# Optimization experiments

Measured on AMD Instinct MI355X. Metric: run time of the kernel, lower is better.

Reference implementation:

```python
import jax, jax.numpy as jnp
import numpy as np

N_NODES = 100000
N_EDGES = 1600000
IN_F = 128
OUT_F = 64
K = 2


def _propagate(x, src, dst, num_nodes):
    """GCN propagation with self-loops already appended to (src, dst).
    out[j] = sum_{(i->j)} deg(i)^-1/2 * deg(j)^-1/2 * x[i]
    where deg is the in-degree counting self-loops (PyG gcn_norm)."""
    deg = jnp.zeros((num_nodes,), dtype=x.dtype).at[dst].add(1.0)
    dinv = jnp.where(deg > 0, jax.lax.rsqrt(deg), 0.0)
    norm = dinv[src] * dinv[dst]                      # [E+N]
    msg = x[src] * norm[:, None]                      # gather + scale
    return jnp.zeros_like(x).at[dst].add(msg)         # scatter-add


def setup_inputs() -> dict:
    key = jax.random.key(0)
    k1, k2, k3, k4 = jax.random.split(key, 4)
    x = jax.random.normal(k1, (N_NODES, IN_F), dtype=jnp.float32)
    edge_index = jax.random.randint(k2, (2, N_EDGES), 0, N_NODES, dtype=jnp.int64)
    # Linear weights, torch convention: y = x @ W.T, W is [out, in]
    W1 = jax.random.normal(k3, (IN_F, IN_F), dtype=jnp.float32) / np.sqrt(IN_F)
    W2 = jax.random.normal(k4, (OUT_F, IN_F), dtype=jnp.float32) / np.sqrt(IN_F)
    return {"x": x, "edge_index": edge_index, "W1": W1, "W2": W2}


def reference(x, edge_index, W1, W2):
    num_nodes = x.shape[0]
    # add self loops once (same augmented edge set used by P1 and P2)
    loop = jnp.arange(num_nodes, dtype=edge_index.dtype)
    src = jnp.concatenate([edge_index[0], loop])
    dst = jnp.concatenate([edge_index[1], loop])
    for _ in range(K):
        x = x @ W1.T
        x = _propagate(x, src, dst, num_nodes)
    x = x @ W2.T
    x = _propagate(x, src, dst, num_nodes)
    # original computes log_softmax into `out` but returns pre-softmax x
    return x
```

## Files before the change

### kernel.cpp

```cpp
#include <hip/hip_runtime.h>

#define NN 100000
#define NE 1600000
#define ENT (NE + NN)
#define NB 196
#define BINCAP 10240


__global__ void probe_zero(const unsigned* __restrict__ edges, int* __restrict__ flag,
                           int* __restrict__ binCnt) {
    int t = threadIdx.x;
    if (t < NB) binCnt[t] = 0;
    if (t == 0) {
        int is64 = 1;
        for (int i = 1; i < 64; i += 2)
            if (edges[i] != 0u) { is64 = 0; break; }
        *flag = is64;
    }
}


__global__ __launch_bounds__(256) void part_kernel(const void* __restrict__ edges,
                                                   const int* __restrict__ flag,
                                                   int* __restrict__ binned,
                                                   int* __restrict__ binCnt) {
    __shared__ int hist[NB], base[NB], rank[NB];
    int t = threadIdx.x;
    for (int i = t; i < NB; i += 256) hist[i] = 0;
    __syncthreads();
    int i0 = blockIdx.x * 4096;
    bool is64 = (*flag != 0);
    int s[16], d[16];
    #pragma unroll
    for (int q = 0; q < 16; ++q) {
        int i = i0 + q * 256 + t;
        if (i < NE) {
            if (is64) {
                s[q] = (int)__builtin_nontemporal_load(&((const long long*)edges)[i]);
                d[q] = (int)__builtin_nontemporal_load(&((const long long*)edges)[NE + i]);
            } else {
                s[q] = __builtin_nontemporal_load(&((const int*)edges)[i]);
                d[q] = __builtin_nontemporal_load(&((const int*)edges)[NE + i]);
            }
            atomicAdd(&hist[d[q] >> 9], 1);
        } else d[q] = -1;
    }
    __syncthreads();
    for (int i = t; i < NB; i += 256) {
        base[i] = atomicAdd(&binCnt[i], hist[i]);
        rank[i] = 0;
    }
    __syncthreads();
    #pragma unroll
    for (int q = 0; q < 16; ++q) {
        if (d[q] >= 0) {
            int b = d[q] >> 9;
            int r = base[b] + atomicAdd(&rank[b], 1);
            if (r < BINCAP)
                binned[(size_t)b * BINCAP + r] = ((d[q] & 511) << 17) | s[q];
        }
    }
}


__global__ __launch_bounds__(1024) void build2_kernel(const int* __restrict__ binCnt,
                                                      const int* __restrict__ binned,
                                                      float* __restrict__ dinv,
                                                      int* __restrict__ rowoff,
                                                      int* __restrict__ edge) {
    extern __shared__ char smem[];
    int* stage = (int*)smem;
    int* hist  = (int*)(smem + (size_t)BINCAP * 4);
    int* sc    = hist + 512;
    int* cur   = sc + 512;
    int* bsc   = cur + 512;
    int b = blockIdx.x, t = threadIdx.x;
    int nb0 = b << 9;
    int nNodes = min(512, NN - nb0);

    if (t < 256) {
        int nodes = (t < NB) ? min(512, NN - (t << 9)) : 0;
        bsc[t] = (t < NB) ? binCnt[t] + nodes : 0;
    }
    if (t < 512) hist[t] = 0;
    __syncthreads();
    for (int off = 1; off < 256; off <<= 1) {
        int a = (t < 256 && t >= off) ? bsc[t - off] : 0;
        __syncthreads();
        if (t < 256) bsc[t] += a;
        __syncthreads();
    }
    int cntRaw = binCnt[b];
    int cnt = min(cntRaw, BINCAP);
    int off0 = bsc[b] - (cntRaw + nNodes);

    const int* e = binned + (size_t)b * BINCAP;
    for (int i = t; i < cnt; i += 1024) atomicAdd(&hist[e[i] >> 17], 1);
    __syncthreads();
    int v = 0;
    if (t < 512) { v = (t < nNodes) ? hist[t] + 1 : 0; sc[t] = v; }
    __syncthreads();
    for (int off = 1; off < 512; off <<= 1) {
        int a = (t < 512 && t >= off) ? sc[t - off] : 0;
        __syncthreads();
        if (t < 512) sc[t] += a;
        __syncthreads();
    }
    if (t < nNodes) {
        dinv[nb0 + t] = rsqrtf((float)(hist[t] + 1));
        int lo = sc[t] - v;
        rowoff[nb0 + t] = off0 + lo;
        stage[lo] = nb0 + t;
        cur[t] = lo + 1;
    }
    if (b == NB - 1 && t == 0) rowoff[NN] = ENT;
    __syncthreads();
    for (int i = t; i < cnt; i += 1024) {
        int pk = e[i];
        int slot = atomicAdd(&cur[pk >> 17], 1);
        if (slot < BINCAP) stage[slot] = pk & 0x1FFFF;
    }
    __syncthreads();
    int total = min(cntRaw + nNodes, BINCAP);
    int* dst = edge + off0;
    for (int i = t; i < total; i += 1024) dst[i] = stage[i];
}


__global__ __launch_bounds__(256) void wprod1_kernel(const float* __restrict__ W1,
                                                     const float* __restrict__ W2,
                                                     float* __restrict__ T) {
    int idx = blockIdx.x * blockDim.x + threadIdx.x;
    if (idx >= 128 * 64) return;
    int k = idx >> 6, j = idx & 63;
    float s = 0.f;
    #pragma unroll 8
    for (int q = 0; q < 128; ++q)
        s += W1[q * 128 + k] * W2[j * 128 + q];
    T[k * 64 + j] = s;
}

__global__ __launch_bounds__(256) void wprod2_kernel(const float* __restrict__ W1,
                                                     const float* __restrict__ T,
                                                     float* __restrict__ WcT) {
    int idx = blockIdx.x * blockDim.x + threadIdx.x;
    if (idx >= 128 * 64) return;
    int i = idx >> 6, j = idx & 63;
    float s = 0.f;
    #pragma unroll 8
    for (int k = 0; k < 128; ++k)
        s += W1[k * 128 + i] * T[k * 64 + j];
    WcT[j * 128 + i] = s;
}


template<int SPOW>
__global__ __launch_bounds__(256) void spmm64f_kernel(const int* __restrict__ rowoff,
                                                      const int* __restrict__ col,
                                                      const float* __restrict__ dinv,
                                                      const float* __restrict__ H,
                                                      float* __restrict__ O) {
    int w = (int)((blockIdx.x * (unsigned)blockDim.x + threadIdx.x) >> 6);
    if (w >= NN) return;
    int lane = threadIdx.x & 63;
    int s = __builtin_amdgcn_readfirstlane(rowoff[w]);
    int e = __builtin_amdgcn_readfirstlane(rowoff[w + 1]);
    float acc = 0.f;
    const float* base = H + lane;

    int p = s;
    for (; p + 8 <= e; p += 8) {
        int c[8];
        #pragma unroll
        for (int q = 0; q < 8; ++q) c[q] = __builtin_nontemporal_load(&col[p + q]);
        #pragma unroll
        for (int q = 0; q < 8; ++q) acc += base[(size_t)c[q] * 64];
    }
    if (p + 4 <= e) {
        int c[4];
        #pragma unroll
        for (int q = 0; q < 4; ++q) c[q] = __builtin_nontemporal_load(&col[p + q]);
        #pragma unroll
        for (int q = 0; q < 4; ++q) acc += base[(size_t)c[q] * 64];
        p += 4;
    }
    for (; p < e; ++p) acc += base[(size_t)__builtin_nontemporal_load(&col[p]) * 64];

    float di = dinv[w];
    float scale = (SPOW == 2) ? di * di : di;
    __builtin_nontemporal_store(acc * scale, &O[(size_t)w * 64 + lane]);
}


__global__ __launch_bounds__(256) void gemm_xwt64_kernel(const float* __restrict__ X,
                                                         const float* __restrict__ W,
                                                         const float* __restrict__ dinv,
                                                         float* __restrict__ Y, int M) {
    constexpr int N = 64, K = 128, BM = 64, BK = 32;
    constexpr int TM = 4, TN = N / 16;
    __shared__ float Xs[BK][BM + 4];
    __shared__ float Ws[BK][N + 4];
    int t  = threadIdx.x;
    int m0 = blockIdx.x * BM;
    int r0 = (t >> 4) * TM;
    int c0 = (t & 15) * TN;
    float acc[TM][TN] = {};
    for (int k0 = 0; k0 < K; k0 += BK) {
        #pragma unroll
        for (int i = 0; i < 2; ++i) {
            int f  = t + i * 256;
            int m  = f >> 3;
            int kq = (f & 7) << 2;
            int gm = m0 + m; if (gm >= M) gm = M - 1;
            float4 v = *(const float4*)&X[(size_t)gm * K + k0 + kq];
            Xs[kq + 0][m] = v.x; Xs[kq + 1][m] = v.y;
            Xs[kq + 2][m] = v.z; Xs[kq + 3][m] = v.w;
        }
        #pragma unroll
        for (int i = 0; i < N / 32; ++i) {
            int f  = t + i * 256;
            int n  = f >> 3;
            int kq = (f & 7) << 2;
            float4 v = *(const float4*)&W[(size_t)n * K + k0 + kq];
            Ws[kq + 0][n] = v.x; Ws[kq + 1][n] = v.y;
            Ws[kq + 2][n] = v.z; Ws[kq + 3][n] = v.w;
        }
        __syncthreads();
        #pragma unroll
        for (int k = 0; k < BK; ++k) {
            float4 xv = *(const float4*)&Xs[k][r0];
            float xf[TM] = {xv.x, xv.y, xv.z, xv.w};
            float wf[TN];
            #pragma unroll
            for (int j = 0; j < TN; j += 4) {
                float4 wv = *(const float4*)&Ws[k][c0 + j];
                wf[j] = wv.x; wf[j + 1] = wv.y; wf[j + 2] = wv.z; wf[j + 3] = wv.w;
            }
            #pragma unroll
            for (int i = 0; i < TM; ++i)
                #pragma unroll
                for (int j = 0; j < TN; ++j)
                    acc[i][j] += xf[i] * wf[j];
        }
        __syncthreads();
    }
    #pragma unroll
    for (int i = 0; i < TM; ++i) {
        int gm = m0 + r0 + i;
        if (gm < M) {
            float di = dinv[gm];
            #pragma unroll
            for (int j = 0; j < TN; j += 4) {
                float4 v = {di * acc[i][j], di * acc[i][j + 1],
                            di * acc[i][j + 2], di * acc[i][j + 3]};
                *(float4*)&Y[(size_t)gm * N + c0 + j] = v;
            }
        }
    }
}


extern "C" void kernel_launch(void* const* d_in, const int* in_sizes, int n_in,
                              void* d_out, int out_size, void* d_ws, size_t ws_size,
                              hipStream_t stream) {
    const float* x     = (const float*)d_in[0];
    const void*  edges = d_in[1];
    const float* W1    = (const float*)d_in[2];
    const float* W2    = (const float*)d_in[3];
    float* out = (float*)d_out;

    char* ws = (char*)d_ws;
    size_t off = 0;
    auto take = [&](size_t bytes) -> char* {
        char* p = ws + off;
        off = (off + bytes + 255) & ~(size_t)255;
        return p;
    };
    int*   flag   = (int*)take(4);
    int*   binCnt = (int*)take((size_t)NB * 4);
    float* dinv   = (float*)take((size_t)NN * 4);
    int*   rowoff = (int*)take((size_t)(NN + 1) * 4);
    float* Tbuf   = (float*)take((size_t)128 * 64 * 4);
    float* WcT    = (float*)take((size_t)64 * 128 * 4);
    int*   binned = (int*)take((size_t)NB * BINCAP * 4);
    int*   edgeA  = (int*)take((size_t)ENT * 4);
    float* g      = (float*)take((size_t)NN * 64 * 4);
    float* y      = (float*)take((size_t)NN * 64 * 4);
    if (off > ws_size) return;

    probe_zero<<<1, 256, 0, stream>>>((const unsigned*)edges, flag, binCnt);
    wprod1_kernel<<<32, 256, 0, stream>>>(W1, W2, Tbuf);
    wprod2_kernel<<<32, 256, 0, stream>>>(W1, Tbuf, WcT);
    part_kernel<<<(NE + 4095) / 4096, 256, 0, stream>>>(edges, flag, binned, binCnt);
    size_t b2lds = (size_t)BINCAP * 4 + (512 * 3 + 256) * 4;
    build2_kernel<<<NB, 1024, b2lds, stream>>>(binCnt, binned, dinv, rowoff, edgeA);

    const int GB = (NN + 63) / 64;
    const int PB = (NN * 64 + 255) / 256;

    gemm_xwt64_kernel<<<GB, 256, 0, stream>>>(x, WcT, dinv, g, NN);
    spmm64f_kernel<2><<<PB, 256, 0, stream>>>(rowoff, edgeA, dinv, g, y);
    spmm64f_kernel<2><<<PB, 256, 0, stream>>>(rowoff, edgeA, dinv, y, g);
    spmm64f_kernel<1><<<PB, 256, 0, stream>>>(rowoff, edgeA, dinv, g, out);
}
```

Baseline: 262.8 us.

## Fuse setup kernels, deepen SpMM unroll, use nontemporal GEMM loads/stores

Merges the probe/zeroing kernel into the first weight-product kernel and folds the second weight product into the tail of the partition kernel, removing two launches. The SpMM row loop is unrolled to 16 gathers in flight, and the GEMM switches its X loads and Y stores to nontemporal scalar accesses. Splitting the float4 accesses into scalars may cost vectorization, and running the weight product inside the partition kernel lengthens a few of its blocks.

```diff
diff --git a/kernel.cpp b/kernel.cpp
--- a/kernel.cpp
+++ b/kernel.cpp
@@ -7,23 +7,40 @@
 #define BINCAP 10240
 
 
-__global__ void probe_zero(const unsigned* __restrict__ edges, int* __restrict__ flag,
-                           int* __restrict__ binCnt) {
-    int t = threadIdx.x;
-    if (t < NB) binCnt[t] = 0;
-    if (t == 0) {
-        int is64 = 1;
-        for (int i = 1; i < 64; i += 2)
-            if (edges[i] != 0u) { is64 = 0; break; }
-        *flag = is64;
-    }
+__global__ __launch_bounds__(256) void wprod1_kernel(const float* __restrict__ W1,
+                                                     const float* __restrict__ W2,
+                                                     float* __restrict__ T,
+                                                     const unsigned* __restrict__ edges,
+                                                     int* __restrict__ flag,
+                                                     int* __restrict__ binCnt) {
+    if (blockIdx.x == 0) {
+        int t = threadIdx.x;
+        if (t < NB) binCnt[t] = 0;
+        if (t == 0) {
+            int is64 = 1;
+            for (int i = 1; i < 64; i += 2)
+                if (edges[i] != 0u) { is64 = 0; break; }
+            *flag = is64;
+        }
+    }
+    int idx = blockIdx.x * blockDim.x + threadIdx.x;
+    if (idx >= 128 * 64) return;
+    int k = idx >> 6, j = idx & 63;
+    float s = 0.f;
+    #pragma unroll 8
+    for (int q = 0; q < 128; ++q)
+        s += W1[q * 128 + k] * W2[j * 128 + q];
+    T[k * 64 + j] = s;
 }
 
 
 __global__ __launch_bounds__(256) void part_kernel(const void* __restrict__ edges,
                                                    const int* __restrict__ flag,
                                                    int* __restrict__ binned,
-                                                   int* __restrict__ binCnt) {
+                                                   int* __restrict__ binCnt,
+                                                   const float* __restrict__ W1,
+                                                   const float* __restrict__ T,
+                                                   float* __restrict__ WcT) {
     __shared__ int hist[NB], base[NB], rank[NB];
     int t = threadIdx.x;
     for (int i = t; i < NB; i += 256) hist[i] = 0;
@@ -60,6 +77,15 @@
                 binned[(size_t)b * BINCAP + r] = ((d[q] & 511) << 17) | s[q];
         }
     }
+    if (blockIdx.x < 32) {
+        int idx = blockIdx.x * 256 + t;
+        int i = idx >> 6, j = idx & 63;
+        float sum = 0.f;
+        #pragma unroll 8
+        for (int k = 0; k < 128; ++k)
+            sum += W1[k * 128 + i] * T[k * 64 + j];
+        WcT[j * 128 + i] = sum;
+    }
 }
 
 
@@ -127,33 +153,6 @@
 }
 
 
-__global__ __launch_bounds__(256) void wprod1_kernel(const float* __restrict__ W1,
-                                                     const float* __restrict__ W2,
-                                                     float* __restrict__ T) {
-    int idx = blockIdx.x * blockDim.x + threadIdx.x;
-    if (idx >= 128 * 64) return;
-    int k = idx >> 6, j = idx & 63;
-    float s = 0.f;
-    #pragma unroll 8
-    for (int q = 0; q < 128; ++q)
-        s += W1[q * 128 + k] * W2[j * 128 + q];
-    T[k * 64 + j] = s;
-}
-
-__global__ __launch_bounds__(256) void wprod2_kernel(const float* __restrict__ W1,
-                                                     const float* __restrict__ T,
-                                                     float* __restrict__ WcT) {
-    int idx = blockIdx.x * blockDim.x + threadIdx.x;
-    if (idx >= 128 * 64) return;
-    int i = idx >> 6, j = idx & 63;
-    float s = 0.f;
-    #pragma unroll 8
-    for (int k = 0; k < 128; ++k)
-        s += W1[k * 128 + i] * T[k * 64 + j];
-    WcT[j * 128 + i] = s;
-}
-
-
 template<int SPOW>
 __global__ __launch_bounds__(256) void spmm64f_kernel(const int* __restrict__ rowoff,
                                                       const int* __restrict__ col,
@@ -169,12 +168,20 @@
     const float* base = H + lane;
 
     int p = s;
-    for (; p + 8 <= e; p += 8) {
+    for (; p + 16 <= e; p += 16) {
+        int c[16];
+        #pragma unroll
+        for (int q = 0; q < 16; ++q) c[q] = __builtin_nontemporal_load(&col[p + q]);
+        #pragma unroll
+        for (int q = 0; q < 16; ++q) acc += base[(size_t)c[q] * 64];
+    }
+    if (p + 8 <= e) {
         int c[8];
         #pragma unroll
         for (int q = 0; q < 8; ++q) c[q] = __builtin_nontemporal_load(&col[p + q]);
         #pragma unroll
         for (int q = 0; q < 8; ++q) acc += base[(size_t)c[q] * 64];
+        p += 8;
     }
     if (p + 4 <= e) {
         int c[4];
@@ -212,7 +219,11 @@
             int m  = f >> 3;
             int kq = (f & 7) << 2;
             int gm = m0 + m; if (gm >= M) gm = M - 1;
-            float4 v = *(const float4*)&X[(size_t)gm * K + k0 + kq];
+            float4 v;
+            v.x = __builtin_nontemporal_load(&X[(size_t)gm * K + k0 + kq + 0]);
+            v.y = __builtin_nontemporal_load(&X[(size_t)gm * K + k0 + kq + 1]);
+            v.z = __builtin_nontemporal_load(&X[(size_t)gm * K + k0 + kq + 2]);
+            v.w = __builtin_nontemporal_load(&X[(size_t)gm * K + k0 + kq + 3]);
             Xs[kq + 0][m] = v.x; Xs[kq + 1][m] = v.y;
             Xs[kq + 2][m] = v.z; Xs[kq + 3][m] = v.w;
         }
@@ -250,11 +261,9 @@
         if (gm < M) {
             float di = dinv[gm];
             #pragma unroll
-            for (int j = 0; j < TN; j += 4) {
-                float4 v = {di * acc[i][j], di * acc[i][j + 1],
-                            di * acc[i][j + 2], di * acc[i][j + 3]};
-                *(float4*)&Y[(size_t)gm * N + c0 + j] = v;
-            }
+            for (int j = 0; j < TN; ++j)
+                __builtin_nontemporal_store(di * acc[i][j],
+                                            &Y[(size_t)gm * N + c0 + j]);
         }
     }
 }
@@ -288,10 +297,9 @@
     float* y      = (float*)take((size_t)NN * 64 * 4);
     if (off > ws_size) return;
 
-    probe_zero<<<1, 256, 0, stream>>>((const unsigned*)edges, flag, binCnt);
-    wprod1_kernel<<<32, 256, 0, stream>>>(W1, W2, Tbuf);
-    wprod2_kernel<<<32, 256, 0, stream>>>(W1, Tbuf, WcT);
-    part_kernel<<<(NE + 4095) / 4096, 256, 0, stream>>>(edges, flag, binned, binCnt);
+    wprod1_kernel<<<32, 256, 0, stream>>>(W1, W2, Tbuf, (const unsigned*)edges, flag, binCnt);
+    part_kernel<<<(NE + 4095) / 4096, 256, 0, stream>>>(edges, flag, binned, binCnt,
+                                                        W1, Tbuf, WcT);
     size_t b2lds = (size_t)BINCAP * 4 + (512 * 3 + 256) * 4;
     build2_kernel<<<NB, 1024, b2lds, stream>>>(binCnt, binned, dinv, rowoff, edgeA);
 
```

After: 254.0 us. -3.3%, faster.
